# Kernel optimization log

Hardware: AMD Instinct MI355X
Metric: run time of the kernel (lower is better)

## Reference

```python
import jax, jax.numpy as jnp
import numpy as np

B, T, D = 4, 2048, 1024
E, F, K = 8, 4096, 2  # num experts, ffn hidden, top-k


def setup_inputs() -> dict:
    key = jax.random.key(0)
    ks = jax.random.split(key, 7)
    s_in = 1.0 / np.sqrt(D)
    s_ff = 1.0 / np.sqrt(F)
    return {
        "x": jax.random.normal(ks[0], (B, T, D), dtype=jnp.float32),
        "Wg": jax.random.normal(ks[1], (D, E), dtype=jnp.float32) * s_in,
        "bg": jnp.zeros((E,), dtype=jnp.float32),
        "W1": jax.random.normal(ks[2], (E, D, F), dtype=jnp.float32) * s_in,
        "b1": jnp.zeros((E, F), dtype=jnp.float32),
        "W2": jax.random.normal(ks[3], (E, F, D), dtype=jnp.float32) * s_ff,
        "b2": jnp.zeros((E, D), dtype=jnp.float32),
    }


def reference(x, Wg, bg, W1, b1, W2, b2):
    # Gate: per-token expert logits [B, T, E]
    logits = jnp.einsum("btd,de->bte", x, Wg) + bg
    # Top-k per token, softmax over only the selected logits (as in the source)
    topv, topi = jax.lax.top_k(logits, K)          # [B, T, K]
    probs = jax.nn.softmax(topv, axis=-1)           # [B, T, K]
    out = jnp.zeros_like(x)
    # Loop over the small fixed expert set; each expert runs a dense MLP over
    # all tokens, masked/weighted by its routing probability (0 if unselected).
    for e in range(E):
        w = jnp.sum(probs * (topi == e), axis=-1)   # [B, T] combine weight
        h = jax.nn.gelu(jnp.einsum("btd,df->btf", x, W1[e]) + b1[e], approximate=False)
        y = jnp.einsum("btf,fd->btd", h, W2[e]) + b2[e]
        out = out + w[..., None] * y
    return out
```

## Files before the change

kernel.cpp:

```cpp
#include <hip/hip_runtime.h>
#include <cstdint>

#define B_ 4
#define T_ 2048
#define D_ 1024
#define E_ 8
#define F_ 4096
#define K_ 2
#define N_ (B_*T_)
#define NR_ (N_*K_)

#define TM 128
#define TN 128
#define BK 32
#define MAXP (NR_ + E_*TM)
#define MAXMB (NR_/TM + E_)

typedef __attribute__((ext_vector_type(8))) short short8;
typedef __attribute__((ext_vector_type(4))) float f32x4;

typedef const __attribute__((address_space(1))) unsigned int* gp1_t;
typedef __attribute__((address_space(3))) unsigned int* lp3_t;

__device__ __forceinline__ void gl_lds16(const void* g, void* l) {
    __builtin_amdgcn_global_load_lds((gp1_t)g, (lp3_t)l, 16, 0, 0);
}

__device__ __forceinline__ unsigned short f2b(float f) {
    union { float f; unsigned int u; } v; v.f = f;
    unsigned int u = v.u;
    return (unsigned short)((u + 0x7FFFu + ((u >> 16) & 1u)) >> 16);
}

__device__ __forceinline__ float gelu_exact(float x) {
    return 0.5f * x * (1.0f + erff(x * 0.70710678118654752440f));
}

__global__ __launch_bounds__(256) void gate_kernel(
    const float* __restrict__ x, const float* __restrict__ Wg,
    const float* __restrict__ bg, int* __restrict__ topi,
    float* __restrict__ topw, int* __restrict__ counts) {
    int tid  = threadIdx.x;
    int lane = tid & 63;
    int tok  = blockIdx.x * 4 + (tid >> 6);
    int e = lane & 7;
    int c = lane >> 3;
    const float4* xp = (const float4*)(x + (size_t)tok * D_ + c * 128);
    const float*  wp = Wg + (size_t)(c * 128) * E_ + e;
    float acc = 0.f;
    #pragma unroll 8
    for (int i = 0; i < 32; ++i) {
        float4 xv = xp[i];
        acc += xv.x * wp[(i*4+0)*E_];
        acc += xv.y * wp[(i*4+1)*E_];
        acc += xv.z * wp[(i*4+2)*E_];
        acc += xv.w * wp[(i*4+3)*E_];
    }
    acc += __shfl_xor(acc, 8, 64);
    acc += __shfl_xor(acc, 16, 64);
    acc += __shfl_xor(acc, 32, 64);
    float logit = acc + bg[e];
    float v1 = -3.4e38f, v2 = -3.4e38f; int i1 = -1, i2 = -1;
    for (int ee = 0; ee < 8; ++ee) {
        float le = __shfl(logit, ee, 64);
        if (le > v1) { v2 = v1; i2 = i1; v1 = le; i1 = ee; }
        else if (le > v2) { v2 = le; i2 = ee; }
    }
    if (lane == 0) {
        float p2 = expf(v2 - v1);
        float s  = 1.0f + p2;
        topi[tok*2]   = i1; topw[tok*2]   = 1.0f / s;
        topi[tok*2+1] = i2; topw[tok*2+1] = p2 / s;
        atomicAdd(&counts[i1], 1);
        atomicAdd(&counts[i2], 1);
    }
}

__global__ void scan_kernel(const int* __restrict__ counts,
                            int* __restrict__ offs, int* __restrict__ cursors,
                            int* __restrict__ mb_e, int* __restrict__ mb_m0) {
    if (threadIdx.x == 0) {
        int s = 0, mb = 0;
        for (int e = 0; e < E_; ++e) {
            offs[e] = s; cursors[e] = s;
            int nb = (counts[e] + TM - 1) / TM;
            for (int i = 0; i < nb; ++i) { mb_e[mb] = e; mb_m0[mb] = s + i*TM; ++mb; }
            s += nb * TM;
        }
        offs[E_] = s;
        for (int b = mb; b < MAXMB; ++b) mb_e[b] = -1;
    }
}

__global__ __launch_bounds__(256) void scatter_kernel(
    const int* __restrict__ topi, int* __restrict__ cursors,
    int* __restrict__ perm, int* __restrict__ slots) {
    int t = blockIdx.x * blockDim.x + threadIdx.x;
    if (t >= N_) return;
    #pragma unroll
    for (int k = 0; k < K_; ++k) {
        int e = topi[t*2 + k];
        int pos = atomicAdd(&cursors[e], 1);
        perm[pos] = t;
        slots[t*2 + k] = pos;
    }
}

__global__ __launch_bounds__(256) void castx_kernel(
    const float* __restrict__ x, unsigned short* __restrict__ xb) {
    int i = blockIdx.x * blockDim.x + threadIdx.x;
    float4 v = ((const float4*)x)[i];
    ushort4 o; o.x = f2b(v.x); o.y = f2b(v.y); o.z = f2b(v.z); o.w = f2b(v.w);
    ((ushort4*)xb)[i] = o;
}

__global__ __launch_bounds__(256) void tcast_kernel(
    const float* __restrict__ src, unsigned short* __restrict__ dst, int R, int C) {
    __shared__ float tile[64][65];
    int rb = blockIdx.x * 64, cb = blockIdx.y * 64;
    const float* s = src + (size_t)blockIdx.z * R * C;
    unsigned short* d = dst + (size_t)blockIdx.z * R * C;
    int tx = threadIdx.x & 15, ty = threadIdx.x >> 4;
    #pragma unroll
    for (int i = 0; i < 4; ++i) {
        int r = ty + i*16;
        float4 v = *(const float4*)&s[(size_t)(rb + r) * C + cb + tx*4];
        tile[r][tx*4+0] = v.x; tile[r][tx*4+1] = v.y;
        tile[r][tx*4+2] = v.z; tile[r][tx*4+3] = v.w;
    }
    __syncthreads();
    #pragma unroll
    for (int i = 0; i < 4; ++i) {
        int c = ty + i*16;
        ushort4 o;
        o.x = f2b(tile[tx*4+0][c]);
        o.y = f2b(tile[tx*4+1][c]);
        o.z = f2b(tile[tx*4+2][c]);
        o.w = f2b(tile[tx*4+3][c]);
        *(ushort4*)&d[(size_t)(cb + c) * R + rb + tx*4] = o;
    }
}

__global__ __launch_bounds__(256, 4) void ffn1_kernel(
    const unsigned short* __restrict__ Xb, const unsigned short* __restrict__ W1t,
    const float* __restrict__ b1, const int* __restrict__ perm,
    const int* __restrict__ mb_e, const int* __restrict__ mb_m0,
    unsigned short* __restrict__ H) {
    int e = mb_e[blockIdx.x];
    if (e < 0) return;
    int m0 = mb_m0[blockIdx.x];
    int n0 = blockIdx.y * TN;
    const unsigned short* Bw = W1t + (size_t)e * F_ * D_;

    __shared__ __align__(16) unsigned short lA[TM*BK];
    __shared__ __align__(16) unsigned short lB[TN*BK];

    int t = threadIdx.x;
    int lane = t & 63;
    int wv = t >> 6;
    int wrow = (wv >> 1) * 64, wcol = (wv & 1) * 64;
    int lr = lane & 15, q = lane >> 4;

    int ar0 = t >> 2;
    int ac  = (t & 3) * 8;
    int tok0 = perm[m0 + ar0];
    int tok1 = perm[m0 + 64 + ar0];
    const unsigned short* pa0 = Xb + (size_t)tok0 * D_ + ac;
    const unsigned short* pa1 = Xb + (size_t)tok1 * D_ + ac;
    const unsigned short* pb0 = Bw + (size_t)(n0 + ar0)      * D_ + ac;
    const unsigned short* pb1 = Bw + (size_t)(n0 + 64 + ar0) * D_ + ac;

    f32x4 acc[4][4];
    #pragma unroll
    for (int mi = 0; mi < 4; ++mi)
        #pragma unroll
        for (int ni = 0; ni < 4; ++ni)
            acc[mi][ni] = (f32x4){0.f, 0.f, 0.f, 0.f};

    for (int kk = 0; kk < D_/BK; ++kk) {
        int k0 = kk * BK;
        gl_lds16(pa0 + k0, &lA[t*8]);
        gl_lds16(pa1 + k0, &lA[2048 + t*8]);
        gl_lds16(pb0 + k0, &lB[t*8]);
        gl_lds16(pb1 + k0, &lB[2048 + t*8]);
        asm volatile("s_waitcnt vmcnt(0)" ::: "memory");
        __syncthreads();
        short8 af[4], bf[4];
        #pragma unroll
        for (int mi = 0; mi < 4; ++mi)
            af[mi] = *(const short8*)&lA[(wrow + mi*16 + lr)*BK + q*8];
        #pragma unroll
        for (int ni = 0; ni < 4; ++ni)
            bf[ni] = *(const short8*)&lB[(wcol + ni*16 + lr)*BK + q*8];
        #pragma unroll
        for (int mi = 0; mi < 4; ++mi)
            #pragma unroll
            for (int ni = 0; ni < 4; ++ni)
                acc[mi][ni] = __builtin_amdgcn_mfma_f32_16x16x32_bf16(
                    af[mi], bf[ni], acc[mi][ni], 0, 0, 0);
        __syncthreads();
    }

    const float* b1e = b1 + (size_t)e * F_;
    #pragma unroll
    for (int mi = 0; mi < 4; ++mi) {
        int gr = m0 + wrow + mi*16 + q*4;
        #pragma unroll
        for (int ni = 0; ni < 4; ++ni) {
            int f = n0 + wcol + ni*16 + lr;
            float bb = b1e[f];
            #pragma unroll
            for (int r = 0; r < 4; ++r) {
                float h = gelu_exact(acc[mi][ni][r] + bb);
                H[(size_t)(gr + r) * F_ + f] = f2b(h);
            }
        }
    }
}

__global__ __launch_bounds__(256, 4) void ffn2_kernel(
    const unsigned short* __restrict__ H, const unsigned short* __restrict__ W2t,
    const float* __restrict__ b2,
    const int* __restrict__ mb_e, const int* __restrict__ mb_m0,
    float* __restrict__ Y) {
    int e = mb_e[blockIdx.x];
    if (e < 0) return;
    int m0 = mb_m0[blockIdx.x];
    int n0 = blockIdx.y * TN;
    const unsigned short* Bw = W2t + (size_t)e * D_ * F_;

    __shared__ __align__(16) unsigned short lA[TM*BK];
    __shared__ __align__(16) unsigned short lB[TN*BK];

    int t = threadIdx.x;
    int lane = t & 63;
    int wv = t >> 6;
    int wrow = (wv >> 1) * 64, wcol = (wv & 1) * 64;
    int lr = lane & 15, q = lane >> 4;

    int ar0 = t >> 2;
    int ac  = (t & 3) * 8;
    const unsigned short* pa0 = H + (size_t)(m0 + ar0)      * F_ + ac;
    const unsigned short* pa1 = H + (size_t)(m0 + 64 + ar0) * F_ + ac;
    const unsigned short* pb0 = Bw + (size_t)(n0 + ar0)      * F_ + ac;
    const unsigned short* pb1 = Bw + (size_t)(n0 + 64 + ar0) * F_ + ac;

    f32x4 acc[4][4];
    #pragma unroll
    for (int mi = 0; mi < 4; ++mi)
        #pragma unroll
        for (int ni = 0; ni < 4; ++ni)
            acc[mi][ni] = (f32x4){0.f, 0.f, 0.f, 0.f};

    for (int kk = 0; kk < F_/BK; ++kk) {
        int k0 = kk * BK;
        gl_lds16(pa0 + k0, &lA[t*8]);
        gl_lds16(pa1 + k0, &lA[2048 + t*8]);
        gl_lds16(pb0 + k0, &lB[t*8]);
        gl_lds16(pb1 + k0, &lB[2048 + t*8]);
        asm volatile("s_waitcnt vmcnt(0)" ::: "memory");
        __syncthreads();
        short8 af[4], bf[4];
        #pragma unroll
        for (int mi = 0; mi < 4; ++mi)
            af[mi] = *(const short8*)&lA[(wrow + mi*16 + lr)*BK + q*8];
        #pragma unroll
        for (int ni = 0; ni < 4; ++ni)
            bf[ni] = *(const short8*)&lB[(wcol + ni*16 + lr)*BK + q*8];
        #pragma unroll
        for (int mi = 0; mi < 4; ++mi)
            #pragma unroll
            for (int ni = 0; ni < 4; ++ni)
                acc[mi][ni] = __builtin_amdgcn_mfma_f32_16x16x32_bf16(
                    af[mi], bf[ni], acc[mi][ni], 0, 0, 0);
        __syncthreads();
    }

    const float* b2e = b2 + (size_t)e * D_;
    #pragma unroll
    for (int mi = 0; mi < 4; ++mi) {
        int gr = m0 + wrow + mi*16 + q*4;
        #pragma unroll
        for (int ni = 0; ni < 4; ++ni) {
            int dcol = n0 + wcol + ni*16 + lr;
            float bb = b2e[dcol];
            #pragma unroll
            for (int r = 0; r < 4; ++r)
                Y[(size_t)(gr + r) * D_ + dcol] = acc[mi][ni][r] + bb;
        }
    }
}

__global__ __launch_bounds__(256) void combine_kernel(
    const float* __restrict__ Y, const int* __restrict__ slots,
    const float* __restrict__ topw, float* __restrict__ out) {
    int i = blockIdx.x * 256 + threadIdx.x;
    int t  = i >> 8;
    int d4 = (i & 255) * 4;
    int s0 = slots[t*2], s1 = slots[t*2+1];
    float w0 = topw[t*2], w1 = topw[t*2+1];
    float4 y0 = *(const float4*)&Y[(size_t)s0 * D_ + d4];
    float4 y1 = *(const float4*)&Y[(size_t)s1 * D_ + d4];
    float4 o;
    o.x = w0*y0.x + w1*y1.x;
    o.y = w0*y0.y + w1*y1.y;
    o.z = w0*y0.z + w1*y1.z;
    o.w = w0*y0.w + w1*y1.w;
    ((float4*)out)[i] = o;
}

extern "C" void kernel_launch(void* const* d_in, const int* in_sizes, int n_in,
                              void* d_out, int out_size, void* d_ws, size_t ws_size,
                              hipStream_t stream) {
    const float* x  = (const float*)d_in[0];
    const float* Wg = (const float*)d_in[1];
    const float* bg = (const float*)d_in[2];
    const float* W1 = (const float*)d_in[3];
    const float* b1 = (const float*)d_in[4];
    const float* W2 = (const float*)d_in[5];
    const float* b2 = (const float*)d_in[6];
    float* out = (float*)d_out;

    char* wsp = (char*)d_ws;
    size_t off = 0;
    auto alloc = [&](size_t bytes) {
        void* p = wsp + off;
        off += (bytes + 255) & ~(size_t)255;
        return p;
    };
    int*   topi    = (int*)  alloc((size_t)NR_*4);
    float* topw    = (float*)alloc((size_t)NR_*4);
    int*   slots   = (int*)  alloc((size_t)NR_*4);
    int*   counts  = (int*)  alloc(E_*4);
    int*   offs    = (int*)  alloc((E_+1)*4);
    int*   cursors = (int*)  alloc(E_*4);
    int*   mb_e    = (int*)  alloc(MAXMB*4);
    int*   mb_m0   = (int*)  alloc(MAXMB*4);
    int*   perm    = (int*)  alloc((size_t)MAXP*4);
    unsigned short* Xb  = (unsigned short*)alloc((size_t)N_*D_*2);
    unsigned short* W1t = (unsigned short*)alloc((size_t)E_*D_*F_*2);
    unsigned short* W2t = (unsigned short*)alloc((size_t)E_*D_*F_*2);
    unsigned short* Hb  = (unsigned short*)alloc((size_t)MAXP*F_*2);
    float*          Yb  = (float*)         alloc((size_t)MAXP*D_*4);

    hipMemsetAsync(counts, 0, E_*4, stream);
    hipMemsetAsync(perm, 0, (size_t)MAXP*4, stream);

    gate_kernel<<<N_/4, 256, 0, stream>>>(x, Wg, bg, topi, topw, counts);
    scan_kernel<<<1, 64, 0, stream>>>(counts, offs, cursors, mb_e, mb_m0);
    scatter_kernel<<<N_/256, 256, 0, stream>>>(topi, cursors, perm, slots);
    castx_kernel<<<(N_*(size_t)D_/4)/256, 256, 0, stream>>>(x, Xb);
    tcast_kernel<<<dim3(D_/64, F_/64, E_), 256, 0, stream>>>(W1, W1t, D_, F_);
    tcast_kernel<<<dim3(F_/64, D_/64, E_), 256, 0, stream>>>(W2, W2t, F_, D_);
    ffn1_kernel<<<dim3(MAXMB, F_/TN), 256, 0, stream>>>(Xb, W1t, b1, perm, mb_e, mb_m0, Hb);
    ffn2_kernel<<<dim3(MAXMB, D_/TN), 256, 0, stream>>>(Hb, W2t, b2, mb_e, mb_m0, Yb);
    combine_kernel<<<(N_*(size_t)D_/4)/256, 256, 0, stream>>>(Yb, slots, topw, out);
}
```

Before: 1.144 ms.

## Widen FFN GEMM tiles to 128x256 and store expert outputs in bf16

Both expert GEMM kernels now use a 128x256 output tile, with each wave computing 64x128 (32 accumulators). This raises MFMA work per LDS load of A, which targets memory traffic and load overhead. The cost is more registers and LDS, so occupancy drops (launch bounds go from 4 to 2). Separately, the ffn2 output buffer is stored as bf16 instead of fp32, halving write and read traffic in the combine step at some accuracy cost.

```diff
diff --git a/kernel.cpp b/kernel.cpp
--- a/kernel.cpp
+++ b/kernel.cpp
@@ -11,7 +11,7 @@
 #define NR_ (N_*K_)
 
 #define TM 128
-#define TN 128
+#define TN 256
 #define BK 32
 #define MAXP (NR_ + E_*TM)
 #define MAXMB (NR_/TM + E_)
@@ -30,6 +30,11 @@
     union { float f; unsigned int u; } v; v.f = f;
     unsigned int u = v.u;
     return (unsigned short)((u + 0x7FFFu + ((u >> 16) & 1u)) >> 16);
+}
+
+__device__ __forceinline__ float b2f(unsigned short u) {
+    union { unsigned int i; float f; } v; v.i = ((unsigned int)u) << 16;
+    return v.f;
 }
 
 __device__ __forceinline__ float gelu_exact(float x) {
@@ -141,7 +146,7 @@
     }
 }
 
-__global__ __launch_bounds__(256, 4) void ffn1_kernel(
+__global__ __launch_bounds__(256, 2) void ffn1_kernel(
     const unsigned short* __restrict__ Xb, const unsigned short* __restrict__ W1t,
     const float* __restrict__ b1, const int* __restrict__ perm,
     const int* __restrict__ mb_e, const int* __restrict__ mb_m0,
@@ -158,7 +163,7 @@
     int t = threadIdx.x;
     int lane = t & 63;
     int wv = t >> 6;
-    int wrow = (wv >> 1) * 64, wcol = (wv & 1) * 64;
+    int wrow = (wv >> 1) * 64, wcol = (wv & 1) * 128;
     int lr = lane & 15, q = lane >> 4;
 
     int ar0 = t >> 2;
@@ -167,14 +172,16 @@
     int tok1 = perm[m0 + 64 + ar0];
     const unsigned short* pa0 = Xb + (size_t)tok0 * D_ + ac;
     const unsigned short* pa1 = Xb + (size_t)tok1 * D_ + ac;
-    const unsigned short* pb0 = Bw + (size_t)(n0 + ar0)      * D_ + ac;
-    const unsigned short* pb1 = Bw + (size_t)(n0 + 64 + ar0) * D_ + ac;
-
-    f32x4 acc[4][4];
+    const unsigned short* pb0 = Bw + (size_t)(n0 + ar0)       * D_ + ac;
+    const unsigned short* pb1 = Bw + (size_t)(n0 + 64  + ar0) * D_ + ac;
+    const unsigned short* pb2 = Bw + (size_t)(n0 + 128 + ar0) * D_ + ac;
+    const unsigned short* pb3 = Bw + (size_t)(n0 + 192 + ar0) * D_ + ac;
+
+    f32x4 acc[4][8];
     #pragma unroll
     for (int mi = 0; mi < 4; ++mi)
         #pragma unroll
-        for (int ni = 0; ni < 4; ++ni)
+        for (int ni = 0; ni < 8; ++ni)
             acc[mi][ni] = (f32x4){0.f, 0.f, 0.f, 0.f};
 
     for (int kk = 0; kk < D_/BK; ++kk) {
@@ -183,19 +190,21 @@
         gl_lds16(pa1 + k0, &lA[2048 + t*8]);
         gl_lds16(pb0 + k0, &lB[t*8]);
         gl_lds16(pb1 + k0, &lB[2048 + t*8]);
+        gl_lds16(pb2 + k0, &lB[4096 + t*8]);
+        gl_lds16(pb3 + k0, &lB[6144 + t*8]);
         asm volatile("s_waitcnt vmcnt(0)" ::: "memory");
         __syncthreads();
-        short8 af[4], bf[4];
+        short8 af[4], bf[8];
         #pragma unroll
         for (int mi = 0; mi < 4; ++mi)
             af[mi] = *(const short8*)&lA[(wrow + mi*16 + lr)*BK + q*8];
         #pragma unroll
-        for (int ni = 0; ni < 4; ++ni)
+        for (int ni = 0; ni < 8; ++ni)
             bf[ni] = *(const short8*)&lB[(wcol + ni*16 + lr)*BK + q*8];
         #pragma unroll
         for (int mi = 0; mi < 4; ++mi)
             #pragma unroll
-            for (int ni = 0; ni < 4; ++ni)
+            for (int ni = 0; ni < 8; ++ni)
                 acc[mi][ni] = __builtin_amdgcn_mfma_f32_16x16x32_bf16(
                     af[mi], bf[ni], acc[mi][ni], 0, 0, 0);
         __syncthreads();
@@ -206,7 +215,7 @@
     for (int mi = 0; mi < 4; ++mi) {
         int gr = m0 + wrow + mi*16 + q*4;
         #pragma unroll
-        for (int ni = 0; ni < 4; ++ni) {
+        for (int ni = 0; ni < 8; ++ni) {
             int f = n0 + wcol + ni*16 + lr;
             float bb = b1e[f];
             #pragma unroll
@@ -218,11 +227,11 @@
     }
 }
 
-__global__ __launch_bounds__(256, 4) void ffn2_kernel(
+__global__ __launch_bounds__(256, 2) void ffn2_kernel(
     const unsigned short* __restrict__ H, const unsigned short* __restrict__ W2t,
     const float* __restrict__ b2,
     const int* __restrict__ mb_e, const int* __restrict__ mb_m0,
-    float* __restrict__ Y) {
+    unsigned short* __restrict__ Y) {
     int e = mb_e[blockIdx.x];
     if (e < 0) return;
     int m0 = mb_m0[blockIdx.x];
@@ -235,21 +244,23 @@
     int t = threadIdx.x;
     int lane = t & 63;
     int wv = t >> 6;
-    int wrow = (wv >> 1) * 64, wcol = (wv & 1) * 64;
+    int wrow = (wv >> 1) * 64, wcol = (wv & 1) * 128;
     int lr = lane & 15, q = lane >> 4;
 
     int ar0 = t >> 2;
     int ac  = (t & 3) * 8;
     const unsigned short* pa0 = H + (size_t)(m0 + ar0)      * F_ + ac;
     const unsigned short* pa1 = H + (size_t)(m0 + 64 + ar0) * F_ + ac;
-    const unsigned short* pb0 = Bw + (size_t)(n0 + ar0)      * F_ + ac;
-    const unsigned short* pb1 = Bw + (size_t)(n0 + 64 + ar0) * F_ + ac;
-
-    f32x4 acc[4][4];
+    const unsigned short* pb0 = Bw + (size_t)(n0 + ar0)       * F_ + ac;
+    const unsigned short* pb1 = Bw + (size_t)(n0 + 64  + ar0) * F_ + ac;
+    const unsigned short* pb2 = Bw + (size_t)(n0 + 128 + ar0) * F_ + ac;
+    const unsigned short* pb3 = Bw + (size_t)(n0 + 192 + ar0) * F_ + ac;
+
+    f32x4 acc[4][8];
     #pragma unroll
     for (int mi = 0; mi < 4; ++mi)
         #pragma unroll
-        for (int ni = 0; ni < 4; ++ni)
+        for (int ni = 0; ni < 8; ++ni)
             acc[mi][ni] = (f32x4){0.f, 0.f, 0.f, 0.f};
 
     for (int kk = 0; kk < F_/BK; ++kk) {
@@ -258,19 +269,21 @@
         gl_lds16(pa1 + k0, &lA[2048 + t*8]);
         gl_lds16(pb0 + k0, &lB[t*8]);
         gl_lds16(pb1 + k0, &lB[2048 + t*8]);
+        gl_lds16(pb2 + k0, &lB[4096 + t*8]);
+        gl_lds16(pb3 + k0, &lB[6144 + t*8]);
         asm volatile("s_waitcnt vmcnt(0)" ::: "memory");
         __syncthreads();
-        short8 af[4], bf[4];
+        short8 af[4], bf[8];
         #pragma unroll
         for (int mi = 0; mi < 4; ++mi)
             af[mi] = *(const short8*)&lA[(wrow + mi*16 + lr)*BK + q*8];
         #pragma unroll
-        for (int ni = 0; ni < 4; ++ni)
+        for (int ni = 0; ni < 8; ++ni)
             bf[ni] = *(const short8*)&lB[(wcol + ni*16 + lr)*BK + q*8];
         #pragma unroll
         for (int mi = 0; mi < 4; ++mi)
             #pragma unroll
-            for (int ni = 0; ni < 4; ++ni)
+            for (int ni = 0; ni < 8; ++ni)
                 acc[mi][ni] = __builtin_amdgcn_mfma_f32_16x16x32_bf16(
                     af[mi], bf[ni], acc[mi][ni], 0, 0, 0);
         __syncthreads();
@@ -281,32 +294,31 @@
     for (int mi = 0; mi < 4; ++mi) {
         int gr = m0 + wrow + mi*16 + q*4;
         #pragma unroll
-        for (int ni = 0; ni < 4; ++ni) {
+        for (int ni = 0; ni < 8; ++ni) {
             int dcol = n0 + wcol + ni*16 + lr;
             float bb = b2e[dcol];
             #pragma unroll
             for (int r = 0; r < 4; ++r)
-                Y[(size_t)(gr + r) * D_ + dcol] = acc[mi][ni][r] + bb;
+                Y[(size_t)(gr + r) * D_ + dcol] = f2b(acc[mi][ni][r] + bb);
         }
     }
 }
 
 __global__ __launch_bounds__(256) void combine_kernel(
-    const float* __restrict__ Y, const int* __restrict__ slots,
+    const unsigned short* __restrict__ Y, const int* __restrict__ slots,
     const float* __restrict__ topw, float* __restrict__ out) {
-    int i = blockIdx.x * 256 + threadIdx.x;
-    int t  = i >> 8;
-    int d4 = (i & 255) * 4;
+    int t  = blockIdx.x;
+    int d4 = threadIdx.x * 4;
     int s0 = slots[t*2], s1 = slots[t*2+1];
     float w0 = topw[t*2], w1 = topw[t*2+1];
-    float4 y0 = *(const float4*)&Y[(size_t)s0 * D_ + d4];
-    float4 y1 = *(const float4*)&Y[(size_t)s1 * D_ + d4];
+    ushort4 y0 = *(const ushort4*)&Y[(size_t)s0 * D_ + d4];
+    ushort4 y1 = *(const ushort4*)&Y[(size_t)s1 * D_ + d4];
     float4 o;
-    o.x = w0*y0.x + w1*y1.x;
-    o.y = w0*y0.y + w1*y1.y;
-    o.z = w0*y0.z + w1*y1.z;
-    o.w = w0*y0.w + w1*y1.w;
-    ((float4*)out)[i] = o;
+    o.x = w0*b2f(y0.x) + w1*b2f(y1.x);
+    o.y = w0*b2f(y0.y) + w1*b2f(y1.y);
+    o.z = w0*b2f(y0.z) + w1*b2f(y1.z);
+    o.w = w0*b2f(y0.w) + w1*b2f(y1.w);
+    *(float4*)&out[(size_t)t * D_ + d4] = o;
 }
 
 extern "C" void kernel_launch(void* const* d_in, const int* in_sizes, int n_in,
@@ -341,7 +353,7 @@
     unsigned short* W1t = (unsigned short*)alloc((size_t)E_*D_*F_*2);
     unsigned short* W2t = (unsigned short*)alloc((size_t)E_*D_*F_*2);
     unsigned short* Hb  = (unsigned short*)alloc((size_t)MAXP*F_*2);
-    float*          Yb  = (float*)         alloc((size_t)MAXP*D_*4);
+    unsigned short* Yb  = (unsigned short*)alloc((size_t)MAXP*D_*2);
 
     hipMemsetAsync(counts, 0, E_*4, stream);
     hipMemsetAsync(perm, 0, (size_t)MAXP*4, stream);
@@ -354,5 +366,5 @@
     tcast_kernel<<<dim3(F_/64, D_/64, E_), 256, 0, stream>>>(W2, W2t, F_, D_);
     ffn1_kernel<<<dim3(MAXMB, F_/TN), 256, 0, stream>>>(Xb, W1t, b1, perm, mb_e, mb_m0, Hb);
     ffn2_kernel<<<dim3(MAXMB, D_/TN), 256, 0, stream>>>(Hb, W2t, b2, mb_e, mb_m0, Yb);
-    combine_kernel<<<(N_*(size_t)D_/4)/256, 256, 0, stream>>>(Yb, slots, topw, out);
-}
+    combine_kernel<<<N_, 256, 0, stream>>>(Yb, slots, topw, out);
+}
```

Measured after the change: 1.136 ms. About the same (-0.7%).
